# Performance work log

Hardware: AMD Instinct MI355X
Metric: run time of the kernel (lower is better)

## Reference

```python
import jax, jax.numpy as jnp
import numpy as np

EMBED_DIM = 1024
NUM_HEADS = 16
HEAD_DIM = EMBED_DIM // NUM_HEADS


def setup_inputs() -> dict:
    key = jax.random.key(0)
    k1, k2, k3, k4 = jax.random.split(key, 4)
    S, B = 2048, 2
    x = jax.random.normal(k1, (S, B, EMBED_DIM), dtype=jnp.float32)
    # xavier_uniform for in_proj_weight [3E, E]
    limit_in = float(np.sqrt(6.0 / (3 * EMBED_DIM + EMBED_DIM)))
    in_proj_weight = jax.random.uniform(k2, (3 * EMBED_DIM, EMBED_DIM), minval=-limit_in, maxval=limit_in, dtype=jnp.float32)
    in_proj_bias = jnp.zeros((3 * EMBED_DIM,), dtype=jnp.float32)
    # out_proj: nn.Linear default init (kaiming-uniform-ish); use uniform of similar scale
    limit_out = float(np.sqrt(1.0 / EMBED_DIM))
    out_proj_weight = jax.random.uniform(k3, (EMBED_DIM, EMBED_DIM), minval=-limit_out, maxval=limit_out, dtype=jnp.float32)
    out_proj_bias = jnp.zeros((EMBED_DIM,), dtype=jnp.float32)
    return {
        "x": x,
        "in_proj_weight": in_proj_weight,
        "in_proj_bias": in_proj_bias,
        "out_proj_weight": out_proj_weight,
        "out_proj_bias": out_proj_bias,
    }


def reference(x, in_proj_weight, in_proj_bias, out_proj_weight, out_proj_bias):
    S, B, E = x.shape
    H, D = NUM_HEADS, HEAD_DIM
    scaling = float(D) ** -0.5
    # fused QKV projection: [S, B, 3E]
    qkv = jnp.einsum("sbe,fe->sbf", x, in_proj_weight) + in_proj_bias
    q, k, v = jnp.split(qkv, 3, axis=-1)
    q = q * scaling
    # [S, B, E] -> [B*H, S, D]
    def to_heads(t):
        return t.reshape(S, B * H, D).transpose(1, 0, 2)
    q, k, v = to_heads(q), to_heads(k), to_heads(v)
    # attention scores [B*H, S, S]
    scores = jnp.einsum("btd,bsd->bts", q, k)
    weights = jax.nn.softmax(scores, axis=-1)
    # dropout p=0.0 -> identity
    attn = jnp.einsum("bts,bsd->btd", weights, v)  # [B*H, S, D]
    attn = attn.transpose(1, 0, 2).reshape(S, B, E)
    out = jnp.einsum("sbe,fe->sbf", attn, out_proj_weight) + out_proj_bias
    return out
```

## Files before the change

kernel.cpp:

```cpp
#include <hip/hip_runtime.h>

typedef __bf16 bf16_t;
typedef __attribute__((ext_vector_type(8))) __bf16 bf16x8;
typedef __attribute__((ext_vector_type(4))) __bf16 bf16x4;
typedef __attribute__((ext_vector_type(4))) float f32x4;
typedef __attribute__((ext_vector_type(16))) float f32x16;
typedef __attribute__((ext_vector_type(2))) unsigned uint2v;

#define MFMA16(a, b, c) __builtin_amdgcn_mfma_f32_16x16x32_bf16((a), (b), (c), 0, 0, 0)
#define MFMA32(a, b, c) __builtin_amdgcn_mfma_f32_32x32x16_bf16((a), (b), (c), 0, 0, 0)
#define LOG2E 1.44269504088896f

__device__ __forceinline__ void async16(const bf16_t* g, bf16_t* l) {
    __builtin_amdgcn_global_load_lds(
        (const __attribute__((address_space(1))) unsigned int*)g,
        (__attribute__((address_space(3))) unsigned int*)l, 16, 0, 0);
}

__device__ __forceinline__ unsigned pack2(float a, float b) {
    union { bf16_t e[2]; unsigned u; } x;
    x.e[0] = (bf16_t)a; x.e[1] = (bf16_t)b;
    return x.u;
}

__device__ __forceinline__ void pl32swap(unsigned& a, unsigned& b) {
    uint2v r = __builtin_amdgcn_permlane32_swap(a, b, false, false);
    a = r[0]; b = r[1];
}

__device__ __forceinline__ void pbar() {
    asm volatile("" ::: "memory");
    __builtin_amdgcn_s_barrier();
    asm volatile("" ::: "memory");
}

__global__ __launch_bounds__(256) void conv3(
    const float* __restrict__ s0, const float* __restrict__ s1,
    const float* __restrict__ s2, bf16_t* __restrict__ dst,
    int n0, int n1)
{
    const int i = (blockIdx.x * 256 + threadIdx.x) * 8;
    const float* src;
    int off;
    if (i < n0)           { src = s0; off = 0; }
    else if (i < n0 + n1) { src = s1; off = n0; }
    else                  { src = s2; off = n0 + n1; }
    const float4 a = *reinterpret_cast<const float4*>(src + i - off);
    const float4 b = *reinterpret_cast<const float4*>(src + i - off + 4);
    bf16x8 o;
    o[0] = (bf16_t)a.x; o[1] = (bf16_t)a.y; o[2] = (bf16_t)a.z; o[3] = (bf16_t)a.w;
    o[4] = (bf16_t)b.x; o[5] = (bf16_t)b.y; o[6] = (bf16_t)b.z; o[7] = (bf16_t)b.w;
    *reinterpret_cast<bf16x8*>(dst + i) = o;
}

__global__ __launch_bounds__(512, 2) void gemm_qkv(
    const bf16_t* __restrict__ W, const bf16_t* __restrict__ X,
    const float* __restrict__ bias, bf16_t* __restrict__ qkv,
    bf16_t* __restrict__ vtp)
{
    constexpr int K = 1024;
    constexpr int NSTEP = K / 64;
    constexpr int AELEM = 192 * 64;
    constexpr int BELEM = 256 * 64;

    __shared__ bf16_t lds[2][AELEM + BELEM];

    const int tid  = threadIdx.x;
    const int lane = tid & 63;
    const int wv   = tid >> 6;
    const int wm   = wv >> 2;
    const int wn   = wv & 3;
    const int l15  = lane & 15;
    const int qd   = lane >> 4;

    const int id = blockIdx.x;
    const int x8 = id & 7, k = id >> 3;
    const int mb = ((k & 1) * 8 + x8) * 256;
    const int fb = (k >> 1) * 192;

    f32x4 acc[6][4] = {};

    auto stage = [&](int set, int k0) {
        bf16_t* Ab = lds[set];
        bf16_t* Bb = lds[set] + AELEM;
#pragma unroll
        for (int t = 0; t < 3; t++) {
            const int p = t * 512 + tid;
            const int r = p >> 3;
            const int c = (p & 7) ^ (r & 7);
            async16(W + (size_t)(fb + r) * K + k0 + c * 8,
                    Ab + (t * 512 + wv * 64) * 8);
        }
#pragma unroll
        for (int t = 0; t < 4; t++) {
            const int p = t * 512 + tid;
            const int r = p >> 3;
            const int c = (p & 7) ^ (r & 7);
            async16(X + (size_t)(mb + r) * K + k0 + c * 8,
                    Bb + (t * 512 + wv * 64) * 8);
        }
    };

    stage(0, 0);
    for (int s = 0; s < NSTEP; s++) {
        const int set = s & 1;
        __syncthreads();
        if (s + 1 < NSTEP) stage(set ^ 1, (s + 1) * 64);

        const bf16_t* Ab = lds[set];
        const bf16_t* Bb = lds[set] + AELEM;

        bf16x8 a0[3][2], a1[3][2], b0[2][2], b1[2][2];

#pragma unroll
        for (int i = 0; i < 3; i++) {
            const int r = wm * 96 + i * 16 + l15;
            a0[i][0] = *reinterpret_cast<const bf16x8*>(
                Ab + r * 64 + ((qd ^ (r & 7)) * 8));
            a0[i][1] = *reinterpret_cast<const bf16x8*>(
                Ab + r * 64 + (((4 + qd) ^ (r & 7)) * 8));
        }
#pragma unroll
        for (int j = 0; j < 2; j++) {
            const int r = wn * 64 + j * 16 + l15;
            b0[j][0] = *reinterpret_cast<const bf16x8*>(
                Bb + r * 64 + ((qd ^ (r & 7)) * 8));
            b0[j][1] = *reinterpret_cast<const bf16x8*>(
                Bb + r * 64 + (((4 + qd) ^ (r & 7)) * 8));
        }
        __builtin_amdgcn_s_setprio(1);
#pragma unroll
        for (int i = 0; i < 3; i++)
#pragma unroll
            for (int j = 0; j < 2; j++) {
                acc[i][j] = MFMA16(a0[i][0], b0[j][0], acc[i][j]);
                acc[i][j] = MFMA16(a0[i][1], b0[j][1], acc[i][j]);
            }
        __builtin_amdgcn_s_setprio(0);
        pbar();

#pragma unroll
        for (int i = 0; i < 3; i++) {
            const int r = wm * 96 + (i + 3) * 16 + l15;
            a1[i][0] = *reinterpret_cast<const bf16x8*>(
                Ab + r * 64 + ((qd ^ (r & 7)) * 8));
            a1[i][1] = *reinterpret_cast<const bf16x8*>(
                Ab + r * 64 + (((4 + qd) ^ (r & 7)) * 8));
        }
        __builtin_amdgcn_s_setprio(1);
#pragma unroll
        for (int i = 0; i < 3; i++)
#pragma unroll
            for (int j = 0; j < 2; j++) {
                acc[i + 3][j] = MFMA16(a1[i][0], b0[j][0], acc[i + 3][j]);
                acc[i + 3][j] = MFMA16(a1[i][1], b0[j][1], acc[i + 3][j]);
            }
        __builtin_amdgcn_s_setprio(0);
        pbar();

#pragma unroll
        for (int j = 0; j < 2; j++) {
            const int r = wn * 64 + (j + 2) * 16 + l15;
            b1[j][0] = *reinterpret_cast<const bf16x8*>(
                Bb + r * 64 + ((qd ^ (r & 7)) * 8));
            b1[j][1] = *reinterpret_cast<const bf16x8*>(
                Bb + r * 64 + (((4 + qd) ^ (r & 7)) * 8));
        }
        __builtin_amdgcn_s_setprio(1);
#pragma unroll
        for (int i = 0; i < 3; i++)
#pragma unroll
            for (int j = 0; j < 2; j++) {
                acc[i + 3][j + 2] = MFMA16(a1[i][0], b1[j][0], acc[i + 3][j + 2]);
                acc[i + 3][j + 2] = MFMA16(a1[i][1], b1[j][1], acc[i + 3][j + 2]);
            }
        __builtin_amdgcn_s_setprio(0);
        pbar();

        __builtin_amdgcn_s_setprio(1);
#pragma unroll
        for (int i = 0; i < 3; i++)
#pragma unroll
            for (int j = 0; j < 2; j++) {
                acc[i][j + 2] = MFMA16(a0[i][0], b1[j][0], acc[i][j + 2]);
                acc[i][j + 2] = MFMA16(a0[i][1], b1[j][1], acc[i][j + 2]);
            }
        __builtin_amdgcn_s_setprio(0);
    }

#pragma unroll
    for (int i = 0; i < 6; i++) {
        const int f0i = fb + wm * 96 + i * 16;
        const int f0  = f0i + qd * 4;
        const float scale = (f0i < 1024) ? 0.125f * LOG2E : 1.0f;
        const bool vblk = (f0i >= 2048);
        float bs[4];
#pragma unroll
        for (int r = 0; r < 4; r++) bs[r] = bias[f0 + r];
#pragma unroll
        for (int j = 0; j < 4; j++) {
            const int m = mb + wn * 64 + j * 16 + l15;
            if (vblk) {
                const int sIdx = m >> 1;
                const int b2   = (m & 1) << 4;
#pragma unroll
                for (int r = 0; r < 4; r++) {
                    const int fv = f0 + r - 2048;
                    vtp[(size_t)((b2 + (fv >> 6)) * 64 + (fv & 63)) * 2048 + sIdx] =
                        (bf16_t)(acc[i][j][r] + bs[r]);
                }
            } else {
                bf16x4 o;
#pragma unroll
                for (int r = 0; r < 4; r++)
                    o[r] = (bf16_t)((acc[i][j][r] + bs[r]) * scale);
                *reinterpret_cast<bf16x4*>(qkv + (size_t)m * 3072 + f0) = o;
            }
        }
    }
}

__global__ __launch_bounds__(512, 2) void gemm_out(
    const bf16_t* __restrict__ W, const bf16_t* __restrict__ X,
    const float* __restrict__ bias, float* __restrict__ out)
{
    constexpr int K = 1024;
    constexpr int NSTEP = K / 64;
    constexpr int AELEM = 64 * 64;
    constexpr int BELEM = 256 * 64;

    __shared__ bf16_t lds[2][AELEM + BELEM];

    const int tid  = threadIdx.x;
    const int lane = tid & 63;
    const int wv   = tid >> 6;
    const int wm   = wv >> 2;
    const int wn   = wv & 3;
    const int l15  = lane & 15;
    const int qd   = lane >> 4;

    const int id = blockIdx.x;
    const int x8 = id & 7, k = id >> 3;
    const int mb = ((k & 1) * 8 + x8) * 256;
    const int fb = (k >> 1) * 64;

    f32x4 acc[2][4] = {};

    auto stage = [&](int set, int k0) {
        bf16_t* Ab = lds[set];
        bf16_t* Bb = lds[set] + AELEM;
        {
            const int p = tid;
            const int r = p >> 3;
            const int c = (p & 7) ^ (r & 7);
            async16(W + (size_t)(fb + r) * K + k0 + c * 8,
                    Ab + (wv * 64) * 8);
        }
#pragma unroll
        for (int t = 0; t < 4; t++) {
            const int p = t * 512 + tid;
            const int r = p >> 3;
            const int c = (p & 7) ^ (r & 7);
            async16(X + (size_t)(mb + r) * K + k0 + c * 8,
                    Bb + (t * 512 + wv * 64) * 8);
        }
    };

    stage(0, 0);
    for (int s = 0; s < NSTEP; s++) {
        const int set = s & 1;
        __syncthreads();
        if (s + 1 < NSTEP) stage(set ^ 1, (s + 1) * 64);

        const bf16_t* Ab = lds[set];
        const bf16_t* Bb = lds[set] + AELEM;

        bf16x8 a[2][2], b0[2][2], b1[2][2];

#pragma unroll
        for (int i = 0; i < 2; i++) {
            const int r = wm * 32 + i * 16 + l15;
            a[i][0] = *reinterpret_cast<const bf16x8*>(
                Ab + r * 64 + ((qd ^ (r & 7)) * 8));
            a[i][1] = *reinterpret_cast<const bf16x8*>(
                Ab + r * 64 + (((4 + qd) ^ (r & 7)) * 8));
        }
#pragma unroll
        for (int j = 0; j < 2; j++) {
            const int r = wn * 64 + j * 16 + l15;
            b0[j][0] = *reinterpret_cast<const bf16x8*>(
                Bb + r * 64 + ((qd ^ (r & 7)) * 8));
            b0[j][1] = *reinterpret_cast<const bf16x8*>(
                Bb + r * 64 + (((4 + qd) ^ (r & 7)) * 8));
        }
        __builtin_amdgcn_s_setprio(1);
#pragma unroll
        for (int i = 0; i < 2; i++)
#pragma unroll
            for (int j = 0; j < 2; j++) {
                acc[i][j] = MFMA16(a[i][0], b0[j][0], acc[i][j]);
                acc[i][j] = MFMA16(a[i][1], b0[j][1], acc[i][j]);
            }
        __builtin_amdgcn_s_setprio(0);
        pbar();

#pragma unroll
        for (int j = 0; j < 2; j++) {
            const int r = wn * 64 + (j + 2) * 16 + l15;
            b1[j][0] = *reinterpret_cast<const bf16x8*>(
                Bb + r * 64 + ((qd ^ (r & 7)) * 8));
            b1[j][1] = *reinterpret_cast<const bf16x8*>(
                Bb + r * 64 + (((4 + qd) ^ (r & 7)) * 8));
        }
        __builtin_amdgcn_s_setprio(1);
#pragma unroll
        for (int i = 0; i < 2; i++)
#pragma unroll
            for (int j = 0; j < 2; j++) {
                acc[i][j + 2] = MFMA16(a[i][0], b1[j][0], acc[i][j + 2]);
                acc[i][j + 2] = MFMA16(a[i][1], b1[j][1], acc[i][j + 2]);
            }
        __builtin_amdgcn_s_setprio(0);
    }

#pragma unroll
    for (int i = 0; i < 2; i++) {
        const int f0 = fb + wm * 32 + i * 16 + qd * 4;
        float bs[4];
#pragma unroll
        for (int r = 0; r < 4; r++) bs[r] = bias[f0 + r];
#pragma unroll
        for (int j = 0; j < 4; j++) {
            const int m = mb + wn * 64 + j * 16 + l15;
            float4 o;
            o.x = acc[i][j][0] + bs[0];
            o.y = acc[i][j][1] + bs[1];
            o.z = acc[i][j][2] + bs[2];
            o.w = acc[i][j][3] + bs[3];
            *reinterpret_cast<float4*>(out + (size_t)m * 1024 + f0) = o;
        }
    }
}

__global__ __launch_bounds__(256, 2) void flash_attn(
    const bf16_t* __restrict__ qkv, const bf16_t* __restrict__ vT,
    bf16_t* __restrict__ attn, int S, int B)
{
    const int E3 = 3072, E = 1024;
    const int bh = blockIdx.x, b = bh >> 4, h = bh & 15;
    const int tid = threadIdx.x, lane = tid & 63, wv = tid >> 6;
    const int qw = wv & 1;
    const int pr = wv >> 1;
    const int l31 = lane & 31, half = lane >> 5;

    __shared__ bf16_t Kt[2][2][64 * 64];
    __shared__ bf16_t Vt[2][2][64 * 64];
    __shared__ float  lsh[2][64];

    const int q0 = blockIdx.y * 128 + qw * 64;

    bf16x8 qf[2][4];
#pragma unroll
    for (int qt = 0; qt < 2; qt++) {
        const bf16_t* qp = qkv + (size_t)((q0 + qt * 32 + l31) * B + b) * E3 + h * 64;
#pragma unroll
        for (int ks = 0; ks < 4; ks++)
            qf[qt][ks] = *reinterpret_cast<const bf16x8*>(qp + ks * 16 + half * 8);
    }

    f32x16 oacc[2][2] = {};
    float lrun[2] = {0.0f, 0.0f};

    auto stage = [&](int set, int kv) {
#pragma unroll
        for (int t = 0; t < 4; t++) {
            const int p = (qw * 4 + t) * 64 + lane;
            const int r = p >> 3, cl = (p & 7) ^ (r & 7);
            async16(qkv + (size_t)((kv + r) * B + b) * E3 + E + h * 64 + cl * 8,
                    &Kt[pr][set][(qw * 4 + t) * 512]);
            async16(vT + (size_t)(bh * 64 + r) * 2048 + kv + cl * 8,
                    &Vt[pr][set][(qw * 4 + t) * 512]);
        }
    };

    const int kvbase = pr * (S / 2);
    const int NIT = S / 128;

    stage(0, kvbase);
    int set = 0;
    for (int it = 0; it < NIT; it++) {
        __syncthreads();
        if (it + 1 < NIT) stage(set ^ 1, kvbase + (it + 1) * 64);

        const bf16_t* K_ = Kt[pr][set];
        const bf16_t* V_ = Vt[pr][set];

        union PF { unsigned u[4]; bf16x8 v; };
        PF pf[2][4];
#pragma unroll
        for (int nt = 0; nt < 2; nt++) {
            const int r = nt * 32 + l31;
            const int r7 = r & 7;
            bf16x8 kf[4];
#pragma unroll
            for (int ks = 0; ks < 4; ks++)
                kf[ks] = *reinterpret_cast<const bf16x8*>(
                    K_ + r * 64 + (((ks * 2 + half) ^ r7) * 8));
#pragma unroll
            for (int qt = 0; qt < 2; qt++) {
                f32x16 st = {};
                __builtin_amdgcn_s_setprio(1);
#pragma unroll
                for (int ks = 0; ks < 4; ks++)
                    st = MFMA32(kf[ks], qf[qt][ks], st);
                __builtin_amdgcn_s_setprio(0);
                float ls = 0.0f;
                unsigned q8[8];
#pragma unroll
                for (int g = 0; g < 4; g++) {
                    const float p0 = __builtin_amdgcn_exp2f(st[4 * g]);
                    const float p1 = __builtin_amdgcn_exp2f(st[4 * g + 1]);
                    const float p2 = __builtin_amdgcn_exp2f(st[4 * g + 2]);
                    const float p3 = __builtin_amdgcn_exp2f(st[4 * g + 3]);
                    ls += (p0 + p1) + (p2 + p3);
                    q8[2 * g]     = pack2(p0, p1);
                    q8[2 * g + 1] = pack2(p2, p3);
                }
                lrun[qt] += ls;
                pl32swap(q8[0], q8[2]); pl32swap(q8[1], q8[3]);
                pl32swap(q8[4], q8[6]); pl32swap(q8[5], q8[7]);
                pf[qt][nt * 2 + 0].u[0] = q8[0]; pf[qt][nt * 2 + 0].u[1] = q8[1];
                pf[qt][nt * 2 + 0].u[2] = q8[2]; pf[qt][nt * 2 + 0].u[3] = q8[3];
                pf[qt][nt * 2 + 1].u[0] = q8[4]; pf[qt][nt * 2 + 1].u[1] = q8[5];
                pf[qt][nt * 2 + 1].u[2] = q8[6]; pf[qt][nt * 2 + 1].u[3] = q8[7];
            }
        }
        __builtin_amdgcn_s_setprio(1);
#pragma unroll
        for (int kn = 0; kn < 4; kn++)
#pragma unroll
            for (int dt = 0; dt < 2; dt++) {
                const int d = dt * 32 + l31;
                bf16x8 vf = *reinterpret_cast<const bf16x8*>(
                    V_ + d * 64 + (((kn * 2 + half) ^ (d & 7)) * 8));
                oacc[0][dt] = MFMA32(vf, pf[0][kn].v, oacc[0][dt]);
                oacc[1][dt] = MFMA32(vf, pf[1][kn].v, oacc[1][dt]);
            }
        __builtin_amdgcn_s_setprio(0);
        set ^= 1;
    }

    __syncthreads();
    float lr[2];
#pragma unroll
    for (int qt = 0; qt < 2; qt++) lr[qt] = lrun[qt] + __shfl_xor(lrun[qt], 32);

    float* fo = reinterpret_cast<float*>(&Kt[0][0][0]) + qw * 4096;

    if (pr == 1) {
#pragma unroll
        for (int qt = 0; qt < 2; qt++) {
            const int ql = qt * 32 + l31;
            lsh[qw][ql] = lr[qt];
#pragma unroll
            for (int dt = 0; dt < 2; dt++)
#pragma unroll
                for (int g = 0; g < 4; g++)
#pragma unroll
                    for (int r = 0; r < 4; r++) {
                        const int d = dt * 32 + g * 8 + half * 4 + r;
                        fo[d * 64 + ql] = oacc[qt][dt][4 * g + r];
                    }
        }
    }
    __syncthreads();
    if (pr == 0) {
#pragma unroll
        for (int qt = 0; qt < 2; qt++) {
            const int ql = qt * 32 + l31;
            const float inv = 1.0f / (lr[qt] + lsh[qw][ql]);
            const int qrow = q0 + qt * 32 + l31;
#pragma unroll
            for (int dt = 0; dt < 2; dt++)
#pragma unroll
                for (int g = 0; g < 4; g++) {
                    bf16x4 o;
#pragma unroll
                    for (int r = 0; r < 4; r++) {
                        const int d = dt * 32 + g * 8 + half * 4 + r;
                        o[r] = (bf16_t)((oacc[qt][dt][4 * g + r] + fo[d * 64 + ql]) * inv);
                    }
                    *reinterpret_cast<bf16x4*>(attn + (size_t)(qrow * B + b) * E +
                                               h * 64 + dt * 32 + g * 8 + half * 4) = o;
                }
        }
    }
}

extern "C" void kernel_launch(void* const* d_in, const int* in_sizes, int n_in,
                              void* d_out, int out_size, void* d_ws, size_t ws_size,
                              hipStream_t stream) {
    const float* x  = (const float*)d_in[0];
    const float* wi = (const float*)d_in[1];
    const float* bi = (const float*)d_in[2];
    const float* wo = (const float*)d_in[3];
    const float* bo = (const float*)d_in[4];
    float* out = (float*)d_out;

    const int S = 2048, B = 2, E = 1024;
    const int M = S * B;

    bf16_t* xb   = (bf16_t*)d_ws;
    bf16_t* wib  = xb  + (size_t)M * E;
    bf16_t* wob  = wib + (size_t)3 * E * E;
    bf16_t* qkv  = wob + (size_t)E * E;
    bf16_t* vT   = qkv + (size_t)M * 3 * E;
    bf16_t* attn = xb;

    const int n0 = M * E, n1 = 3 * E * E, n2 = E * E;
    conv3<<<(n0 + n1 + n2) / 8 / 256, 256, 0, stream>>>(x, wi, wo, xb, n0, n1);

    gemm_qkv<<<256, 512, 0, stream>>>(wib, xb, bi, qkv, vT);

    flash_attn<<<dim3(B * 16, S / 128), 256, 0, stream>>>(qkv, vT, attn, S, B);

    gemm_out<<<256, 512, 0, stream>>>(wob, attn, bo, out);
}
```

Baseline: 177.7 us.

## Store V in MFMA fragment layout and load it directly into registers

The QKV GEMM epilogue now writes V in a blocked layout matching the MFMA operand fragment order, one 64-key tile per contiguous 4096-element chunk. The attention kernel drops its V shared-memory staging and reads V fragments straight from global memory into registers each iteration. This removes V's LDS traffic and halves LDS use, but the V loads are now synchronous global loads, no longer prefetched, and launch bounds are relaxed to one block per SM to allow more registers. Scattered 2-byte epilogue stores remain.

```diff
diff --git a/kernel.cpp b/kernel.cpp
--- a/kernel.cpp
+++ b/kernel.cpp
@@ -203,10 +203,15 @@
             if (vblk) {
                 const int sIdx = m >> 1;
                 const int b2   = (m & 1) << 4;
+                const int t    = sIdx >> 6;
+                const int ch   = (sIdx >> 3) & 7;
+                const int k0   = sIdx & 7;
 #pragma unroll
                 for (int r = 0; r < 4; r++) {
                     const int fv = f0 + r - 2048;
-                    vtp[(size_t)((b2 + (fv >> 6)) * 64 + (fv & 63)) * 2048 + sIdx] =
+                    const int bh = b2 + (fv >> 6);
+                    const int d  = fv & 63;
+                    vtp[(size_t)(bh * 32 + t) * 4096 + ch * 512 + d * 8 + k0] =
                         (bf16_t)(acc[i][j][r] + bs[r]);
                 }
             } else {
@@ -342,8 +347,8 @@
     }
 }
 
-__global__ __launch_bounds__(256, 2) void flash_attn(
-    const bf16_t* __restrict__ qkv, const bf16_t* __restrict__ vT,
+__global__ __launch_bounds__(256, 1) void flash_attn(
+    const bf16_t* __restrict__ qkv, const bf16_t* __restrict__ vF,
     bf16_t* __restrict__ attn, int S, int B)
 {
     const int E3 = 3072, E = 1024;
@@ -354,7 +359,6 @@
     const int l31 = lane & 31, half = lane >> 5;
 
     __shared__ bf16_t Kt[2][2][64 * 64];
-    __shared__ bf16_t Vt[2][2][64 * 64];
     __shared__ float  lsh[2][64];
 
     const int q0 = blockIdx.y * 128 + qw * 64;
@@ -371,29 +375,36 @@
     f32x16 oacc[2][2] = {};
     float lrun[2] = {0.0f, 0.0f};
 
-    auto stage = [&](int set, int kv) {
+    auto stageK = [&](int set_, int kv) {
 #pragma unroll
         for (int t = 0; t < 4; t++) {
             const int p = (qw * 4 + t) * 64 + lane;
             const int r = p >> 3, cl = (p & 7) ^ (r & 7);
             async16(qkv + (size_t)((kv + r) * B + b) * E3 + E + h * 64 + cl * 8,
-                    &Kt[pr][set][(qw * 4 + t) * 512]);
-            async16(vT + (size_t)(bh * 64 + r) * 2048 + kv + cl * 8,
-                    &Vt[pr][set][(qw * 4 + t) * 512]);
+                    &Kt[pr][set_][(qw * 4 + t) * 512]);
         }
     };
 
     const int kvbase = pr * (S / 2);
     const int NIT = S / 128;
-
-    stage(0, kvbase);
+    const bf16_t* Vhead = vF + (size_t)(bh * 32) * 4096;
+
+    stageK(0, kvbase);
     int set = 0;
     for (int it = 0; it < NIT; it++) {
         __syncthreads();
-        if (it + 1 < NIT) stage(set ^ 1, kvbase + (it + 1) * 64);
+        if (it + 1 < NIT) stageK(set ^ 1, kvbase + (it + 1) * 64);
+
+        const bf16_t* Vg = Vhead + (size_t)(pr * 16 + it) * 4096;
+        bf16x8 vfr[4][2];
+#pragma unroll
+        for (int kn = 0; kn < 4; kn++)
+#pragma unroll
+            for (int dt = 0; dt < 2; dt++)
+                vfr[kn][dt] = *reinterpret_cast<const bf16x8*>(
+                    Vg + (kn * 2 + half) * 512 + (dt * 32 + l31) * 8);
 
         const bf16_t* K_ = Kt[pr][set];
-        const bf16_t* V_ = Vt[pr][set];
 
         union PF { unsigned u[4]; bf16x8 v; };
         PF pf[2][4];
@@ -440,11 +451,8 @@
         for (int kn = 0; kn < 4; kn++)
 #pragma unroll
             for (int dt = 0; dt < 2; dt++) {
-                const int d = dt * 32 + l31;
-                bf16x8 vf = *reinterpret_cast<const bf16x8*>(
-                    V_ + d * 64 + (((kn * 2 + half) ^ (d & 7)) * 8));
-                oacc[0][dt] = MFMA32(vf, pf[0][kn].v, oacc[0][dt]);
-                oacc[1][dt] = MFMA32(vf, pf[1][kn].v, oacc[1][dt]);
+                oacc[0][dt] = MFMA32(vfr[kn][dt], pf[0][kn].v, oacc[0][dt]);
+                oacc[1][dt] = MFMA32(vfr[kn][dt], pf[1][kn].v, oacc[1][dt]);
             }
         __builtin_amdgcn_s_setprio(0);
         set ^= 1;
@@ -514,15 +522,15 @@
     bf16_t* wib  = xb  + (size_t)M * E;
     bf16_t* wob  = wib + (size_t)3 * E * E;
     bf16_t* qkv  = wob + (size_t)E * E;
-    bf16_t* vT   = qkv + (size_t)M * 3 * E;
+    bf16_t* vF   = qkv + (size_t)M * 3 * E;
     bf16_t* attn = xb;
 
     const int n0 = M * E, n1 = 3 * E * E, n2 = E * E;
     conv3<<<(n0 + n1 + n2) / 8 / 256, 256, 0, stream>>>(x, wi, wo, xb, n0, n1);
 
-    gemm_qkv<<<256, 512, 0, stream>>>(wib, xb, bi, qkv, vT);
-
-    flash_attn<<<dim3(B * 16, S / 128), 256, 0, stream>>>(qkv, vT, attn, S, B);
+    gemm_qkv<<<256, 512, 0, stream>>>(wib, xb, bi, qkv, vF);
+
+    flash_attn<<<dim3(B * 16, S / 128), 256, 0, stream>>>(qkv, vF, attn, S, B);
 
     gemm_out<<<256, 512, 0, stream>>>(wob, attn, bo, out);
 }
```

Result: slower. 200.7 us (+12.9%).
